# Performance work log

Hardware: AMD Instinct MI355X
Metric: run time of the kernel (lower is better)

The kernel has to match this reference:

```python
import jax, jax.numpy as jnp
import numpy as np

# geomloss SamplesLoss(loss='sinkhorn', p=2, reach=1.0, blur=0.1) constants
P = 2
BLUR = 0.1
REACH = 1.0
SCALING = 0.5
EPS_FINAL = BLUR ** P          # 0.01
RHO = REACH ** P               # 1.0
DIAMETER = 2.0 * np.sqrt(2.0)  # PMT positions scaled to [-1,1]^2


def eps_schedule():
    # geomloss epsilon_schedule(p, diameter, blur, scaling)
    e = [DIAMETER ** P]
    for t in np.arange(P * np.log(DIAMETER), P * np.log(BLUR), P * np.log(SCALING)):
        e.append(float(np.exp(t)))
    e.append(BLUR ** P)
    return [float(v) for v in e]


def _softmin(eps, C, h):
    # h: (B, N) log-measure + potential/eps ; C: (N, N) shared cost -> (B, N)
    return -eps * jax.scipy.special.logsumexp(h[:, None, :] - C[None, :, :] / eps, axis=-1)


def _sinkhorn_potentials(a_log, b_log, C):
    # symmetric unbalanced Sinkhorn loop with eps-annealing (geomloss sinkhorn_loop)
    eps_list = eps_schedule()
    damp = lambda eps: 1.0 / (1.0 + eps / RHO)
    eps0 = eps_list[0]
    d0 = damp(eps0)
    g_ab = d0 * _softmin(eps0, C, a_log)
    f_ba = d0 * _softmin(eps0, C, b_log)
    f_aa = d0 * _softmin(eps0, C, a_log)
    g_bb = d0 * _softmin(eps0, C, b_log)
    for eps in eps_list:
        d = damp(eps)
        ft = d * _softmin(eps, C, b_log + g_ab / eps)
        gt = d * _softmin(eps, C, a_log + f_ba / eps)
        f_ba, g_ab = 0.5 * (f_ba + ft), 0.5 * (g_ab + gt)
        f_aa = 0.5 * (f_aa + d * _softmin(eps, C, a_log + f_aa / eps))
        g_bb = 0.5 * (g_bb + d * _softmin(eps, C, b_log + g_bb / eps))
    # last extrapolation at the final (target) temperature
    eps = eps_list[-1]
    d = damp(eps)
    f_ba, g_ab = (d * _softmin(eps, C, b_log + g_ab / eps),
                  d * _softmin(eps, C, a_log + f_ba / eps))
    f_aa = d * _softmin(eps, C, a_log + f_aa / eps)
    g_bb = d * _softmin(eps, C, b_log + g_bb / eps)
    return f_aa, g_bb, g_ab, f_ba


def setup_inputs() -> dict:
    key = jax.random.key(0)
    k1, k2, k3 = jax.random.split(key, 3)
    B, N = 32768, 32
    # positive PE weights (measure masses must be > 0 for log-domain Sinkhorn)
    pred_pmtpe = jax.random.uniform(k1, (B, N), jnp.float32, 0.05, 1.0)
    target_pe = jax.random.uniform(k2, (B, N), jnp.float32, 0.05, 1.0)
    # fixed scaled 2D (z,y) PMT layout in [-1,1]^2, shared by pred and target clouds
    pmt_pos = jax.random.uniform(k3, (N, 2), jnp.float32, -1.0, 1.0)
    batchstart = jnp.arange(B, dtype=jnp.int64) * N
    batchend = batchstart + N
    return {"pred_pmtpe": pred_pmtpe, "target_pe": target_pe, "pmt_pos": pmt_pos,
            "batchstart": batchstart, "batchend": batchend}


def reference(pred_pmtpe, target_pe, pmt_pos, batchstart, batchend):
    # shared cost matrix (x_pred_batch == y_target_batch == PMT layout), C = |x-y|^2/2 for p=2
    C = 0.5 * jnp.sum((pmt_pos[:, None, :] - pmt_pos[None, :, :]) ** 2, axis=-1)  # (32,32)
    # geomloss runs the Sinkhorn loop with autograd disabled (envelope theorem)
    a_log = jnp.log(jax.lax.stop_gradient(pred_pmtpe))
    b_log = jnp.log(jax.lax.stop_gradient(target_pe))
    f_aa, g_bb, g_ab, f_ba = _sinkhorn_potentials(a_log, b_log, C)
    f_aa, g_bb, g_ab, f_ba = map(jax.lax.stop_gradient, (f_aa, g_bb, g_ab, f_ba))
    # unbalanced debiased sinkhorn cost (geomloss sinkhorn_cost, rho finite)
    eps = EPS_FINAL
    scale = RHO + 0.5 * eps
    per_batch = scale * (
        jnp.sum(pred_pmtpe * (jnp.exp(-f_aa / RHO) - jnp.exp(-f_ba / RHO)), axis=-1)
        + jnp.sum(target_pe * (jnp.exp(-g_bb / RHO) - jnp.exp(-g_ab / RHO)), axis=-1)
    )
    return jnp.mean(per_batch)
```

## Files before the change

### kernel.cpp

```cpp
#include <hip/hip_runtime.h>

#define EXP2F(x)  __builtin_amdgcn_exp2f(x)
#define LOG2FD(x) __builtin_amdgcn_logf(x)
#define L2E 1.4426950408889634f
#define T1F 1.2621774e-29f

typedef __attribute__((ext_vector_type(8)))  short bf16x8;
typedef __attribute__((ext_vector_type(16))) float f32x16;
typedef __attribute__((ext_vector_type(2)))  unsigned int u32x2;

#define MFMA32(A, B, C) __builtin_amdgcn_mfma_f32_32x32x16_bf16((A), (B), (C), 0, 0, 0)

union U8 { unsigned int u[4]; bf16x8 v; };

__device__ __forceinline__ void split_pack(const float* w, bf16x8& hi, bf16x8& lo) {
  U8 a, b;
#pragma unroll
  for (int k = 0; k < 4; ++k) {
    float x0 = w[2*k], x1 = w[2*k+1];
    unsigned u0 = __float_as_uint(x0) & 0xFFFF0000u;
    unsigned u1 = __float_as_uint(x1) & 0xFFFF0000u;
    float r0 = x0 - __uint_as_float(u0);
    float r1 = x1 - __uint_as_float(u1);
    a.u[k] = (u0 >> 16) | u1;
    b.u[k] = ((__float_as_uint(r0) & 0xFFFF0000u) >> 16) |
             (__float_as_uint(r1) & 0xFFFF0000u);
  }
  hi = a.v; lo = b.v;
}

__device__ __forceinline__ void plswap(float& a, float& b) {
  u32x2 r = __builtin_amdgcn_permlane32_swap(__float_as_uint(a), __float_as_uint(b),
                                             false, false);
  a = __uint_as_float(r.x);
  b = __uint_as_float(r.y);
}

__device__ __noinline__ float exact_lse(const float2* pos2, const float* HB,
                                        int i, float inv) {
  float2 pi = pos2[i];
  float m = -3.4e38f;
#pragma unroll 1
  for (int j = 0; j < 32; ++j) {
    float2 pj = pos2[j];
    float dx = pi.x - pj.x, dy = pi.y - pj.y;
    float arg = fmaf((0.5f*L2E)*(dx*dx + dy*dy), -inv, HB[j]);
    m = fmaxf(m, arg);
  }
  float s = 0.f;
#pragma unroll 1
  for (int j = 0; j < 32; ++j) {
    float2 pj = pos2[j];
    float dx = pi.x - pj.x, dy = pi.y - pj.y;
    float arg = fmaf((0.5f*L2E)*(dx*dx + dy*dy), -inv, HB[j]);
    s += EXP2F(arg - m);
  }
  return m + LOG2FD(s);
}

__device__ __forceinline__ void buildK32(const float* c2, float inv,
                                         bf16x8* KH, bf16x8* KL) {
  float k0[8], k1[8];
#pragma unroll
  for (int e = 0; e < 8; ++e) {
    k0[e] = EXP2F(-c2[e]     * inv);
    k1[e] = EXP2F(-c2[8 + e] * inv);
  }
  split_pack(k0, KH[0], KL[0]);
  split_pack(k1, KH[1], KL[1]);
}

__device__ __forceinline__ void ksoft32(float* out, const float* H,
    const bf16x8* KH, const bf16x8* KL, float nde, float inv,
    bool checked, bool avg, float* Hdump, int lane, const float2* pos2) {
  float t0 = fmaxf(fmaxf(H[0],  H[1]),  fmaxf(H[2],  H[3]));
  float t1 = fmaxf(fmaxf(H[4],  H[5]),  fmaxf(H[6],  H[7]));
  float t2 = fmaxf(fmaxf(H[8],  H[9]),  fmaxf(H[10], H[11]));
  float t3 = fmaxf(fmaxf(H[12], H[13]), fmaxf(H[14], H[15]));
  float mx = fmaxf(fmaxf(t0, t1), fmaxf(t2, t3));
  u32x2 mr = __builtin_amdgcn_permlane32_swap(__float_as_uint(mx), __float_as_uint(mx),
                                              false, false);
  const float hm = fmaxf(__uint_as_float(mr.x), __uint_as_float(mr.y));

  float d[16];
#pragma unroll
  for (int e = 0; e < 16; ++e) d[e] = H[e] - hm;
#pragma unroll
  for (int r = 0; r < 4; ++r) { plswap(d[r], d[4+r]); plswap(d[8+r], d[12+r]); }

  float w[16];
#pragma unroll
  for (int e = 0; e < 16; ++e) w[e] = EXP2F(d[e]);
  bf16x8 w10, w20, w11, w21;
  split_pack(w,     w10, w20);
  split_pack(w + 8, w11, w21);

  f32x16 z;
#pragma unroll
  for (int r = 0; r < 16; ++r) z[r] = 0.f;
  f32x16 a = MFMA32(KH[0], w10, z);
  a = MFMA32(KH[1], w11, a);
  f32x16 b = MFMA32(KL[0], w10, z);
  b = MFMA32(KL[1], w11, b);
  b = MFMA32(KH[0], w20, b);
  b = MFMA32(KH[1], w21, b);

  float S[16], raw[16];
#pragma unroll
  for (int r = 0; r < 16; ++r) S[r] = a[r] + b[r];
#pragma unroll
  for (int r = 0; r < 16; ++r) raw[r] = hm + LOG2FD(S[r]);

  if (checked) {
    float mn = S[0];
#pragma unroll
    for (int r = 1; r < 16; ++r) mn = fminf(mn, S[r]);
    if (__any(mn < T1F)) {
      float wb[16];
#pragma unroll
      for (int e = 0; e < 16; ++e) wb[e] = EXP2F(d[e] + 96.f);
      bf16x8 u10, u20, u11, u21;
      split_pack(wb,     u10, u20);
      split_pack(wb + 8, u11, u21);
      f32x16 p = MFMA32(KH[0], u10, z);
      p = MFMA32(KH[1], u11, p);
      f32x16 q = MFMA32(KL[0], u10, z);
      q = MFMA32(KL[1], u11, q);
      q = MFMA32(KH[0], u20, q);
      q = MFMA32(KH[1], u21, q);
      bool mybad = false;
      float Sb[16];
#pragma unroll
      for (int r = 0; r < 16; ++r) {
        Sb[r] = p[r] + q[r];
        if (S[r] < T1F) raw[r] = (hm - 96.f) + LOG2FD(Sb[r]);
        mybad |= (S[r] < T1F) && (Sb[r] < T1F);
      }
      if (__any(mybad)) {
        const int b31 = lane & 31, hi = lane >> 5;
        float* HB = &Hdump[b31 * 36];
        float4 h0 = {d[0]+hm,  d[1]+hm,  d[2]+hm,  d[3]+hm};
        float4 h1 = {d[4]+hm,  d[5]+hm,  d[6]+hm,  d[7]+hm};
        float4 h2 = {d[8]+hm,  d[9]+hm,  d[10]+hm, d[11]+hm};
        float4 h3 = {d[12]+hm, d[13]+hm, d[14]+hm, d[15]+hm};
        *(float4*)&HB[8*hi]      = h0;
        *(float4*)&HB[8*hi + 4]  = h1;
        *(float4*)&HB[16 + 8*hi]     = h2;
        *(float4*)&HB[16 + 8*hi + 4] = h3;
        asm volatile("" ::: "memory");
#pragma unroll
        for (int r = 0; r < 16; ++r) {
          if ((S[r] < T1F) && (Sb[r] < T1F)) {
            int i = (r & 3) + 8 * (r >> 2) + 4 * hi;
            raw[r] = exact_lse(pos2, HB, i, inv);
          }
        }
      }
    }
  }
#pragma unroll
  for (int r = 0; r < 16; ++r) {
    float v = nde * raw[r];
    out[r] = avg ? 0.5f * (out[r] + v) : v;
  }
}

__global__ __launch_bounds__(64) void sink_kernel(
    const float* __restrict__ pred, const float* __restrict__ tgt,
    const float* __restrict__ pos, float* __restrict__ ws) {
  __shared__ __align__(16) float sHd[32 * 36];

  const int lane = threadIdx.x;
  const int b31  = lane & 31;
  const int hi   = lane >> 5;
  const int bbase = blockIdx.x * 32;
  const float2* pos2 = (const float2*)pos;

  float al2[16], bl2[16];
  {
    const float* pr = &pred[(bbase + b31) * 32 + 4 * hi];
    const float* tr = &tgt [(bbase + b31) * 32 + 4 * hi];
#pragma unroll
    for (int q = 0; q < 4; ++q) {
      float4 pv = *(const float4*)&pr[8 * q];
      float4 tv = *(const float4*)&tr[8 * q];
      al2[4*q+0] = LOG2FD(pv.x); al2[4*q+1] = LOG2FD(pv.y);
      al2[4*q+2] = LOG2FD(pv.z); al2[4*q+3] = LOG2FD(pv.w);
      bl2[4*q+0] = LOG2FD(tv.x); bl2[4*q+1] = LOG2FD(tv.y);
      bl2[4*q+2] = LOG2FD(tv.z); bl2[4*q+3] = LOG2FD(tv.w);
    }
  }
  float c2[16];
  {
    float2 pi = pos2[b31];
#pragma unroll
    for (int f = 0; f < 2; ++f)
#pragma unroll
      for (int e = 0; e < 8; ++e) {
        float2 pj = pos2[16*f + 8*hi + e];
        float dx = pi.x - pj.x, dy = pi.y - pj.y;
        c2[8*f + e] = (0.5f*L2E) * (dx*dx + dy*dy);
      }
  }

  bf16x8 KH[2], KL[2];
  float Fba[16], Gab[16], Faa[16], Gbb[16];

  buildK32(c2, 0.125f, KH, KL);
  ksoft32(Gab, al2, KH, KL, -8.f/9.f, 0.125f, false, false, sHd, lane, pos2);
  ksoft32(Fba, bl2, KH, KL, -8.f/9.f, 0.125f, false, false, sHd, lane, pos2);
#pragma unroll
  for (int r = 0; r < 16; ++r) { Faa[r] = Gab[r]; Gbb[r] = Fba[r]; }

  const float INV[8] = {0.125f, 0.125f, 0.5f, 2.f, 8.f, 32.f, 100.f, 100.f};
  const float NDE[8] = {-8.f/9.f, -8.f/9.f, -2.f/3.f, -1.f/3.f, -1.f/9.f,
                        -1.f/33.f, -1.f/101.f, -1.f/101.f};
  float curInv = 0.125f;
#pragma unroll 1
  for (int k = 0; k < 8; ++k) {
    const float inv = INV[k], nde = NDE[k];
    if (inv != curInv) { buildK32(c2, inv, KH, KL); curInv = inv; }
    const bool checked = (k >= 5);
    const bool avg     = (k < 7);
    float Hf[16], Hg[16];
#pragma unroll
    for (int r = 0; r < 16; ++r) {
      Hf[r] = fmaf(Gab[r], inv, bl2[r]);
      Hg[r] = fmaf(Fba[r], inv, al2[r]);
    }
    ksoft32(Fba, Hf, KH, KL, nde, inv, checked, avg, sHd, lane, pos2);
    ksoft32(Gab, Hg, KH, KL, nde, inv, checked, avg, sHd, lane, pos2);
#pragma unroll
    for (int r = 0; r < 16; ++r) Hf[r] = fmaf(Faa[r], inv, al2[r]);
    ksoft32(Faa, Hf, KH, KL, nde, inv, checked, avg, sHd, lane, pos2);
#pragma unroll
    for (int r = 0; r < 16; ++r) Hf[r] = fmaf(Gbb[r], inv, bl2[r]);
    ksoft32(Gbb, Hf, KH, KL, nde, inv, checked, avg, sHd, lane, pos2);
  }

  float part = 0.f;
#pragma unroll
  for (int r = 0; r < 16; ++r) {
    float pv = EXP2F(al2[r]), tv = EXP2F(bl2[r]);
    part += pv * (EXP2F(-Faa[r]) - EXP2F(-Fba[r]))
          + tv * (EXP2F(-Gbb[r]) - EXP2F(-Gab[r]));
  }
  u32x2 pr2 = __builtin_amdgcn_permlane32_swap(__float_as_uint(part), __float_as_uint(part),
                                               false, false);
  part = __uint_as_float(pr2.x) + __uint_as_float(pr2.y);
  part += __shfl_xor(part, 16);
  part += __shfl_xor(part, 8);
  part += __shfl_xor(part, 4);
  part += __shfl_xor(part, 2);
  part += __shfl_xor(part, 1);
  if (lane == 0) ws[blockIdx.x] = part;
}

__global__ __launch_bounds__(256) void reduce_kernel(
    const float* __restrict__ ws, float* __restrict__ out, int n, float scale) {
  float s = 0.f;
  for (int i = threadIdx.x; i < n; i += 256) s += ws[i];
  s += __shfl_xor(s, 32);
  s += __shfl_xor(s, 16);
  s += __shfl_xor(s, 8);
  s += __shfl_xor(s, 4);
  s += __shfl_xor(s, 2);
  s += __shfl_xor(s, 1);
  __shared__ float a[4];
  if ((threadIdx.x & 63) == 0) a[threadIdx.x >> 6] = s;
  __syncthreads();
  if (threadIdx.x == 0) out[0] = ((a[0] + a[1]) + (a[2] + a[3])) * scale;
}

extern "C" void kernel_launch(void* const* d_in, const int* in_sizes, int n_in,
                              void* d_out, int out_size, void* d_ws, size_t ws_size,
                              hipStream_t stream) {
  const float* pred = (const float*)d_in[0];
  const float* tgt  = (const float*)d_in[1];
  const float* pos  = (const float*)d_in[2];
  const int B = in_sizes[0] / 32;
  const int nblocks = B / 32;
  float* ws = (float*)d_ws;

  sink_kernel<<<nblocks, 64, 0, stream>>>(pred, tgt, pos, ws);
  reduce_kernel<<<1, 256, 0, stream>>>(ws, (float*)d_out, nblocks,
                                       1.005f / (float)B);
}
```

Before: 31.42 us.

## Split cross and self Sinkhorn potentials across separate blocks; break MFMA accumulation chain

Each batch tile is now handled by two blocks. One computes the cross potentials (Fba/Gab) and the other the debiasing self potentials (Faa/Gbb), so the grid doubles and each wave's serial chain of softmin calls halves. The low-order MFMA products are accumulated into a third independent accumulator, which shortens the dependent MFMA chain. The cost is loading inputs and building the kernel matrix twice per tile, plus a second launch-bounds hint asking for two blocks per unit.

```diff
diff --git a/kernel.cpp b/kernel.cpp
--- a/kernel.cpp
+++ b/kernel.cpp
@@ -102,12 +102,12 @@
   a = MFMA32(KH[1], w11, a);
   f32x16 b = MFMA32(KL[0], w10, z);
   b = MFMA32(KL[1], w11, b);
-  b = MFMA32(KH[0], w20, b);
-  b = MFMA32(KH[1], w21, b);
+  f32x16 c = MFMA32(KH[0], w20, z);
+  c = MFMA32(KH[1], w21, c);
 
   float S[16], raw[16];
 #pragma unroll
-  for (int r = 0; r < 16; ++r) S[r] = a[r] + b[r];
+  for (int r = 0; r < 16; ++r) S[r] = (a[r] + b[r]) + c[r];
 #pragma unroll
   for (int r = 0; r < 16; ++r) raw[r] = hm + LOG2FD(S[r]);
 
@@ -126,13 +126,13 @@
       p = MFMA32(KH[1], u11, p);
       f32x16 q = MFMA32(KL[0], u10, z);
       q = MFMA32(KL[1], u11, q);
-      q = MFMA32(KH[0], u20, q);
-      q = MFMA32(KH[1], u21, q);
+      f32x16 o = MFMA32(KH[0], u20, z);
+      o = MFMA32(KH[1], u21, o);
       bool mybad = false;
       float Sb[16];
 #pragma unroll
       for (int r = 0; r < 16; ++r) {
-        Sb[r] = p[r] + q[r];
+        Sb[r] = (p[r] + q[r]) + o[r];
         if (S[r] < T1F) raw[r] = (hm - 96.f) + LOG2FD(Sb[r]);
         mybad |= (S[r] < T1F) && (Sb[r] < T1F);
       }
@@ -165,7 +165,7 @@
   }
 }
 
-__global__ __launch_bounds__(64) void sink_kernel(
+__global__ __launch_bounds__(64, 2) void sink_kernel(
     const float* __restrict__ pred, const float* __restrict__ tgt,
     const float* __restrict__ pos, float* __restrict__ ws) {
   __shared__ __align__(16) float sHd[32 * 36];
@@ -173,7 +173,8 @@
   const int lane = threadIdx.x;
   const int b31  = lane & 31;
   const int hi   = lane >> 5;
-  const int bbase = blockIdx.x * 32;
+  const int bbase = (blockIdx.x >> 1) * 32;
+  const bool cross = (blockIdx.x & 1) == 0;
   const float2* pos2 = (const float2*)pos;
 
   float al2[16], bl2[16];
@@ -204,13 +205,11 @@
   }
 
   bf16x8 KH[2], KL[2];
-  float Fba[16], Gab[16], Faa[16], Gbb[16];
+  float X[16], Y[16];
 
   buildK32(c2, 0.125f, KH, KL);
-  ksoft32(Gab, al2, KH, KL, -8.f/9.f, 0.125f, false, false, sHd, lane, pos2);
-  ksoft32(Fba, bl2, KH, KL, -8.f/9.f, 0.125f, false, false, sHd, lane, pos2);
-#pragma unroll
-  for (int r = 0; r < 16; ++r) { Faa[r] = Gab[r]; Gbb[r] = Fba[r]; }
+  ksoft32(Y, al2, KH, KL, -8.f/9.f, 0.125f, false, false, sHd, lane, pos2);
+  ksoft32(X, bl2, KH, KL, -8.f/9.f, 0.125f, false, false, sHd, lane, pos2);
 
   const float INV[8] = {0.125f, 0.125f, 0.5f, 2.f, 8.f, 32.f, 100.f, 100.f};
   const float NDE[8] = {-8.f/9.f, -8.f/9.f, -2.f/3.f, -1.f/3.f, -1.f/9.f,
@@ -222,29 +221,28 @@
     if (inv != curInv) { buildK32(c2, inv, KH, KL); curInv = inv; }
     const bool checked = (k >= 5);
     const bool avg     = (k < 7);
-    float Hf[16], Hg[16];
+    float HX[16], HY[16];
 #pragma unroll
     for (int r = 0; r < 16; ++r) {
-      Hf[r] = fmaf(Gab[r], inv, bl2[r]);
-      Hg[r] = fmaf(Fba[r], inv, al2[r]);
+      float xin = cross ? Y[r] : X[r];
+      float yin = cross ? X[r] : Y[r];
+      HX[r] = fmaf(xin, inv, bl2[r]);
+      HY[r] = fmaf(yin, inv, al2[r]);
     }
-    ksoft32(Fba, Hf, KH, KL, nde, inv, checked, avg, sHd, lane, pos2);
-    ksoft32(Gab, Hg, KH, KL, nde, inv, checked, avg, sHd, lane, pos2);
-#pragma unroll
-    for (int r = 0; r < 16; ++r) Hf[r] = fmaf(Faa[r], inv, al2[r]);
-    ksoft32(Faa, Hf, KH, KL, nde, inv, checked, avg, sHd, lane, pos2);
-#pragma unroll
-    for (int r = 0; r < 16; ++r) Hf[r] = fmaf(Gbb[r], inv, bl2[r]);
-    ksoft32(Gbb, Hf, KH, KL, nde, inv, checked, avg, sHd, lane, pos2);
+    ksoft32(X, HX, KH, KL, nde, inv, checked, avg, sHd, lane, pos2);
+    ksoft32(Y, HY, KH, KL, nde, inv, checked, avg, sHd, lane, pos2);
   }
 
   float part = 0.f;
 #pragma unroll
   for (int r = 0; r < 16; ++r) {
     float pv = EXP2F(al2[r]), tv = EXP2F(bl2[r]);
-    part += pv * (EXP2F(-Faa[r]) - EXP2F(-Fba[r]))
-          + tv * (EXP2F(-Gbb[r]) - EXP2F(-Gab[r]));
-  }
+    float u = cross ? pv : tv;
+    float v = cross ? tv : pv;
+    part += u * EXP2F(-X[r]) + v * EXP2F(-Y[r]);
+  }
+  if (cross) part = -part;
+
   u32x2 pr2 = __builtin_amdgcn_permlane32_swap(__float_as_uint(part), __float_as_uint(part),
                                                false, false);
   part = __uint_as_float(pr2.x) + __uint_as_float(pr2.y);
@@ -279,7 +277,7 @@
   const float* tgt  = (const float*)d_in[1];
   const float* pos  = (const float*)d_in[2];
   const int B = in_sizes[0] / 32;
-  const int nblocks = B / 32;
+  const int nblocks = (B / 32) * 2;
   float* ws = (float*)d_ws;
 
   sink_kernel<<<nblocks, 64, 0, stream>>>(pred, tgt, pos, ws);
```

Result: slower. 33.46 us (+6.5%).
